# Optimization experiments

Measured on AMD Instinct MI355X. Metric: run time of the kernel, lower is better.

Reference implementation:

```python
import jax, jax.numpy as jnp
import numpy as np

B, L, D = 8, 2048, 1024
LN_EPS = 1e-5
WKV_EPS = 1e-8


def _ln(x, g, b):
    m = x.mean(-1, keepdims=True)
    v = x.var(-1, keepdims=True)  # biased var, matches torch LayerNorm
    return (x - m) * jax.lax.rsqrt(v + LN_EPS) * g + b


def _shift(x):
    # ZeroPad2d((0,0,1,-1)): x_prev[:, t] = x[:, t-1], x_prev[:, 0] = 0
    return jnp.pad(x, ((0, 0), (1, 0), (0, 0)))[:, :-1]


def _wkv(k, v, time_decay, time_first):
    # Faithful to the torch loop: t=0 uses exp(u + k0); t>0 decays prior state
    # (including the u-boosted first term) by exp(-exp(time_decay)).
    ew = jnp.exp(-jnp.exp(time_decay))  # [D]
    e0 = jnp.exp(time_first + k[:, 0])  # [B, D]
    a0 = e0 * v[:, 0]
    b0 = e0

    def step(carry, kv):
        a, b = carry
        kt, vt = kv
        ek = jnp.exp(kt)
        a = ew * a + ek * vt
        b = ew * b + ek
        return (a, b), a / (b + WKV_EPS)

    xs = (jnp.swapaxes(k[:, 1:], 0, 1), jnp.swapaxes(v[:, 1:], 0, 1))  # [L-1, B, D]
    _, outs = jax.lax.scan(step, (a0, b0), xs)
    out0 = (a0 / (b0 + WKV_EPS))[:, None]  # [B, 1, D]
    return jnp.concatenate([out0, jnp.swapaxes(outs, 0, 1)], axis=1)  # [B, L, D]


def setup_inputs() -> dict:
    key = jax.random.key(0)
    ks = jax.random.split(key, 10)
    s = 1.0 / np.sqrt(D)

    def w(k, shape, scale):
        return jax.random.normal(k, shape, jnp.float32) * scale

    return {
        "x": jax.random.normal(ks[0], (B, L, D), jnp.float32),
        "ln1_g": jnp.ones((D,), jnp.float32),
        "ln1_b": jnp.zeros((D,), jnp.float32),
        "Wk": w(ks[1], (D, D), s),
        "Wv": w(ks[2], (D, D), s),
        "Wr": w(ks[3], (D, D), s),
        "Wo": w(ks[4], (D, D), s),
        "time_decay": w(ks[5], (D,), 0.1),
        "time_first": w(ks[6], (D,), 0.1),
        "mix_k": jnp.full((D,), 0.5, jnp.float32),
        "mix_v": jnp.full((D,), 0.5, jnp.float32),
        "mix_r": jnp.full((D,), 0.5, jnp.float32),
        "ln2_g": jnp.ones((D,), jnp.float32),
        "ln2_b": jnp.zeros((D,), jnp.float32),
        "Wfk": w(ks[7], (D, 4 * D), s),
        "Wfv": w(ks[8], (4 * D, D), 1.0 / np.sqrt(4 * D)),
        "Wfr": w(ks[9], (D, D), s),
    }


def reference(x, ln1_g, ln1_b, Wk, Wv, Wr, Wo, time_decay, time_first,
              mix_k, mix_v, mix_r, ln2_g, ln2_b, Wfk, Wfv, Wfr):
    # --- time mixing ---
    xn = _ln(x, ln1_g, ln1_b)
    xp = _shift(xn)
    k = (xn * mix_k + xp * (1.0 - mix_k)) @ Wk
    v = (xn * mix_v + xp * (1.0 - mix_v)) @ Wv
    r = jax.nn.sigmoid((xn * mix_r + xp * (1.0 - mix_r)) @ Wr)
    wkv = _wkv(k, v, time_decay, time_first)
    x = x + (r * wkv) @ Wo
    # --- channel mixing ---
    yn = _ln(x, ln2_g, ln2_b)
    yp = _shift(yn)
    kk = jnp.square(jax.nn.relu((0.5 * yn + 0.5 * yp) @ Wfk))
    rr = jax.nn.sigmoid(yn @ Wfr)
    return x + rr * (kk @ Wfv)
```

## Files before the change

### kernel.cpp

```cpp
#include <hip/hip_runtime.h>
#include <hip/hip_bf16.h>
#include <stdint.h>

typedef __hip_bfloat16 bf16_t;
typedef __attribute__((ext_vector_type(8))) short bf16x8;
typedef __attribute__((ext_vector_type(4))) float f32x4;

#define DEV static __device__ __forceinline__

constexpr int kBB = 8, kL = 2048, kD = 1024;
constexpr int kM = kBB * kL;
constexpr int kSeg = 32, kP = 64;

DEV float bf2f(unsigned short u) { return __uint_as_float((unsigned)u << 16); }
DEV unsigned short f2bf(float f) {
  unsigned u = __float_as_uint(f);
  return (unsigned short)((u + 0x7fffu + ((u >> 16) & 1u)) >> 16);
}

DEV void gld16(const void* g, void* l) {
  const __attribute__((address_space(1))) unsigned* gp =
      (const __attribute__((address_space(1))) unsigned*)(uintptr_t)g;
  __attribute__((address_space(3))) unsigned* lp =
      (__attribute__((address_space(3))) unsigned*)(unsigned)(uintptr_t)l;
  __builtin_amdgcn_global_load_lds(gp, lp, 16, 0, 0);
}

__global__ __launch_bounds__(256) void k_transpose_cast(
    const float* __restrict__ W, bf16_t* __restrict__ Wt, int R, int C) {
  __shared__ float tile[32][33];
  const int bx = blockIdx.x * 32;
  const int by = blockIdx.y * 32;
  const int tx = threadIdx.x & 31, ty = threadIdx.x >> 5;
#pragma unroll
  for (int i = 0; i < 32; i += 8)
    tile[ty + i][tx] = W[(size_t)(by + ty + i) * C + (bx + tx)];
  __syncthreads();
#pragma unroll
  for (int i = 0; i < 32; i += 8)
    Wt[(size_t)(bx + ty + i) * R + (by + tx)] = __float2bfloat16(tile[tx][ty + i]);
}

__global__ __launch_bounds__(256) void k_ln_stats(
    const float* __restrict__ X, float* __restrict__ mean, float* __restrict__ rstd) {
  const int row = blockIdx.x * 4 + (threadIdx.x >> 6);
  const int lane = threadIdx.x & 63;
  const float4* xr = (const float4*)(X + (size_t)row * kD);
  float s = 0.f, s2 = 0.f;
#pragma unroll
  for (int i = 0; i < 4; ++i) {
    float4 v = xr[lane + 64 * i];
    s += v.x + v.y + v.z + v.w;
    s2 += v.x * v.x + v.y * v.y + v.z * v.z + v.w * v.w;
  }
#pragma unroll
  for (int off = 32; off > 0; off >>= 1) {
    s += __shfl_xor(s, off);
    s2 += __shfl_xor(s2, off);
  }
  if (lane == 0) {
    float m = s * (1.f / kD);
    float var = fmaxf(s2 * (1.f / kD) - m * m, 0.f);
    mean[row] = m;
    rstd[row] = rsqrtf(var + 1e-5f);
  }
}

__global__ __launch_bounds__(256) void k_ln_mix1(
    const float* __restrict__ X, const float* __restrict__ mean, const float* __restrict__ rstd,
    const float* __restrict__ g, const float* __restrict__ be,
    const float* __restrict__ mk, const float* __restrict__ mv, const float* __restrict__ mr,
    bf16_t* __restrict__ ok, bf16_t* __restrict__ ov, bf16_t* __restrict__ orr) {
  const int row = blockIdx.x;
  const int l = row & (kL - 1);
  const int i = threadIdx.x;
  const bool hp = (l != 0);
  const float m0 = mean[row], s0 = rstd[row];
  const float m1 = hp ? mean[row - 1] : 0.f;
  const float s1 = hp ? rstd[row - 1] : 0.f;
  float xa[4], pa[4] = {0.f, 0.f, 0.f, 0.f}, ga[4], ba[4], ka[4], va[4], ra[4];
  *(float4*)xa = ((const float4*)(X + (size_t)row * kD))[i];
  if (hp) *(float4*)pa = ((const float4*)(X + (size_t)(row - 1) * kD))[i];
  *(float4*)ga = ((const float4*)g)[i];
  *(float4*)ba = ((const float4*)be)[i];
  *(float4*)ka = ((const float4*)mk)[i];
  *(float4*)va = ((const float4*)mv)[i];
  *(float4*)ra = ((const float4*)mr)[i];
  ushort4 uk, uv, ur;
  unsigned short* pk = (unsigned short*)&uk;
  unsigned short* pv = (unsigned short*)&uv;
  unsigned short* pr = (unsigned short*)&ur;
#pragma unroll
  for (int c = 0; c < 4; ++c) {
    float xn = (xa[c] - m0) * s0 * ga[c] + ba[c];
    float xp = hp ? (pa[c] - m1) * s1 * ga[c] + ba[c] : 0.f;
    pk[c] = f2bf(xn * ka[c] + xp * (1.f - ka[c]));
    pv[c] = f2bf(xn * va[c] + xp * (1.f - va[c]));
    pr[c] = f2bf(xn * ra[c] + xp * (1.f - ra[c]));
  }
  ((ushort4*)(ok + (size_t)row * kD))[i] = uk;
  ((ushort4*)(ov + (size_t)row * kD))[i] = uv;
  ((ushort4*)(orr + (size_t)row * kD))[i] = ur;
}

__global__ __launch_bounds__(256) void k_ln_mix2(
    const float* __restrict__ X, const float* __restrict__ mean, const float* __restrict__ rstd,
    const float* __restrict__ g, const float* __restrict__ be,
    bf16_t* __restrict__ om, bf16_t* __restrict__ on) {
  const int row = blockIdx.x;
  const int l = row & (kL - 1);
  const int i = threadIdx.x;
  const bool hp = (l != 0);
  const float m0 = mean[row], s0 = rstd[row];
  const float m1 = hp ? mean[row - 1] : 0.f;
  const float s1 = hp ? rstd[row - 1] : 0.f;
  float xa[4], pa[4] = {0.f, 0.f, 0.f, 0.f}, ga[4], ba[4];
  *(float4*)xa = ((const float4*)(X + (size_t)row * kD))[i];
  if (hp) *(float4*)pa = ((const float4*)(X + (size_t)(row - 1) * kD))[i];
  *(float4*)ga = ((const float4*)g)[i];
  *(float4*)ba = ((const float4*)be)[i];
  ushort4 um, un;
  unsigned short* qm = (unsigned short*)&um;
  unsigned short* qn = (unsigned short*)&un;
#pragma unroll
  for (int c = 0; c < 4; ++c) {
    float yn = (xa[c] - m0) * s0 * ga[c] + ba[c];
    float yp = hp ? (pa[c] - m1) * s1 * ga[c] + ba[c] : 0.f;
    qm[c] = f2bf(0.5f * (yn + yp));
    qn[c] = f2bf(yn);
  }
  ((ushort4*)(om + (size_t)row * kD))[i] = um;
  ((ushort4*)(on + (size_t)row * kD))[i] = un;
}

__global__ __launch_bounds__(256) void k_wkv_seg(
    const unsigned short* __restrict__ kq, const unsigned short* __restrict__ vq,
    const float* __restrict__ td, const float* __restrict__ tf,
    float* __restrict__ segA, float* __restrict__ segB) {
  const int d = blockIdx.x * 256 + threadIdx.x;
  const int b = blockIdx.y;
  const int s = blockIdx.z;
  const float ew = __expf(-__expf(td[d]));
  const float uu = (s == 0) ? tf[d] : 0.f;
  const size_t base = ((size_t)b * kL + (size_t)s * kP) * kD + d;
  float a = 0.f, bb = 0.f;
  unsigned short kA[16], vA[16], kB[16], vB[16];
  auto pref = [&](unsigned short* ka, unsigned short* va, int c) {
    const size_t o0 = base + (size_t)c * 16 * kD;
#pragma unroll
    for (int j = 0; j < 16; ++j) {
      ka[j] = kq[o0 + (size_t)j * kD];
      va[j] = vq[o0 + (size_t)j * kD];
    }
  };
  auto comp = [&](const unsigned short* ka, const unsigned short* va, int c) {
#pragma unroll
    for (int j = 0; j < 16; ++j) {
      float kf = bf2f(ka[j]);
      if (s == 0 && c == 0 && j == 0) kf += uu;
      float ek = __expf(kf);
      a = ew * a + ek * bf2f(va[j]);
      bb = ew * bb + ek;
    }
  };
  pref(kA, vA, 0);
  pref(kB, vB, 1); comp(kA, vA, 0);
  pref(kA, vA, 2); comp(kB, vB, 1);
  pref(kB, vB, 3); comp(kA, vA, 2);
  comp(kB, vB, 3);
  const size_t sidx = ((size_t)b * kSeg + s) * kD + d;
  segA[sidx] = a;
  segB[sidx] = bb;
}

__global__ __launch_bounds__(256) void k_wkv_carry(
    const float* __restrict__ td,
    const float* __restrict__ segA, const float* __restrict__ segB,
    float* __restrict__ carA, float* __restrict__ carB) {
  const int d = blockIdx.x * 256 + threadIdx.x;
  const int b = blockIdx.y;
  const float ew = __expf(-__expf(td[d]));
  float ewP = ew;
#pragma unroll
  for (int i = 0; i < 6; ++i) ewP *= ewP;
  float ca = 0.f, cb = 0.f;
#pragma unroll 4
  for (int s = 0; s < kSeg; ++s) {
    const size_t idx = ((size_t)b * kSeg + s) * kD + d;
    carA[idx] = ca;
    carB[idx] = cb;
    ca = ewP * ca + segA[idx];
    cb = ewP * cb + segB[idx];
  }
}

__global__ __launch_bounds__(256) void k_wkv_out(
    const unsigned short* __restrict__ kq, const unsigned short* __restrict__ vq,
    const unsigned short* __restrict__ rq, const float* __restrict__ td,
    const float* __restrict__ tf, const float* __restrict__ carA,
    const float* __restrict__ carB, unsigned short* __restrict__ out) {
  const int d = blockIdx.x * 256 + threadIdx.x;
  const int b = blockIdx.y;
  const int s = blockIdx.z;
  const float ew = __expf(-__expf(td[d]));
  const float uu = (s == 0) ? tf[d] : 0.f;
  const size_t base = ((size_t)b * kL + (size_t)s * kP) * kD + d;
  const size_t sidx = ((size_t)b * kSeg + s) * kD + d;
  float a = carA[sidx], bb = carB[sidx];
  unsigned short kA[16], vA[16], rA[16], kB[16], vB[16], rB[16];
  auto pref = [&](unsigned short* ka, unsigned short* va, unsigned short* ra, int c) {
    const size_t o0 = base + (size_t)c * 16 * kD;
#pragma unroll
    for (int j = 0; j < 16; ++j) {
      ka[j] = kq[o0 + (size_t)j * kD];
      va[j] = vq[o0 + (size_t)j * kD];
      ra[j] = rq[o0 + (size_t)j * kD];
    }
  };
  auto comp = [&](const unsigned short* ka, const unsigned short* va,
                  const unsigned short* ra, int c) {
    const size_t o0 = base + (size_t)c * 16 * kD;
#pragma unroll
    for (int j = 0; j < 16; ++j) {
      float kf = bf2f(ka[j]);
      if (s == 0 && c == 0 && j == 0) kf += uu;
      float ek = __expf(kf);
      a = ew * a + ek * bf2f(va[j]);
      bb = ew * bb + ek;
      float y = a / (bb + 1e-8f);
      float sr = 1.f / (1.f + __expf(-bf2f(ra[j])));
      out[o0 + (size_t)j * kD] = f2bf(sr * y);
    }
  };
  pref(kA, vA, rA, 0);
  pref(kB, vB, rB, 1); comp(kA, vA, rA, 0);
  pref(kA, vA, rA, 2); comp(kB, vB, rB, 1);
  pref(kB, vB, rB, 3); comp(kA, vA, rA, 2);
  comp(kB, vB, rB, 3);
}

template <int EPI>
__global__ __launch_bounds__(512, 2) void gemmT(
    const bf16_t* __restrict__ A0, long strA, int lda,
    const bf16_t* __restrict__ B0, long strB, int ldb,
    bf16_t* __restrict__ Cb0, float* __restrict__ Cf, long strC,
    int N, int K, int nbx,
    const float* __restrict__ addf, const bf16_t* __restrict__ mulb) {
  __shared__ __align__(16) char lds[131072];
  const int z = blockIdx.z;
  const bf16_t* A = A0 + (size_t)z * strA;
  const bf16_t* Bt = B0 + (size_t)z * strB;
  const int nwg = gridDim.x;
  const int wg = (blockIdx.x & 7) * (nwg >> 3) + (blockIdx.x >> 3);
  const int by = wg / nbx, bx = wg - by * nbx;
  const long brow = (long)by * 256;
  const long bcol = (long)bx * 256;
  const int tid = threadIdx.x;
  const int lane = tid & 63;
  const int wid = tid >> 6;
  const int wr = wid >> 2, wc = wid & 3;

  f32x4 acc[8][4] = {};

  const int trow = tid >> 3;
  const int scol = ((tid & 7) * 16) ^ ((trow & 7) << 4);
  const char* Ag = (const char*)(A + (brow + trow) * (size_t)lda) + scol;
  const char* Bg = (const char*)(Bt + (bcol + trow) * (size_t)ldb) + scol;
  const long rsA = 64L * lda * 2;
  const long rsB = 64L * ldb * 2;

#define STAGE(kt, p)                                   \
  {                                                    \
    const long kb = (long)(kt) * 128;                  \
    char* Ld = lds + (p) * 65536 + tid * 16;           \
    gld16(Ag + kb, Ld);                                \
    gld16(Ag + kb + rsA, Ld + 8192);                   \
    gld16(Ag + kb + 2 * rsA, Ld + 16384);              \
    gld16(Ag + kb + 3 * rsA, Ld + 24576);              \
    gld16(Bg + kb, Ld + 32768);                        \
    gld16(Bg + kb + rsB, Ld + 40960);                  \
    gld16(Bg + kb + 2 * rsB, Ld + 49152);              \
    gld16(Bg + kb + 3 * rsB, Ld + 57344);              \
  }

  const int l16 = lane & 15, kq = lane >> 4;
  const int swz = (l16 & 7) << 4;
  const int oS0 = (kq * 16) ^ swz;
  const int oS1 = (64 + kq * 16) ^ swz;
  const char* Arow = lds + (wr * 128 + l16) * 128;
  const char* Brow = lds + 32768 + (wc * 64 + l16) * 128;

  bf16x8 aE[8], bE[4], aO[8], bO[4];
  const int NT = K >> 6;

  STAGE(0, 0) STAGE(1, 1)
  asm volatile("s_waitcnt vmcnt(8)" ::: "memory");
  __builtin_amdgcn_s_barrier();
#pragma unroll
  for (int m = 0; m < 8; ++m) aE[m] = *(const bf16x8*)(Arow + m * 2048 + oS0);
#pragma unroll
  for (int n = 0; n < 4; ++n) bE[n] = *(const bf16x8*)(Brow + n * 2048 + oS0);

  for (int t = 0; t < NT; ++t) {
    const int p = t & 1;
    const char* Ap = Arow + p * 65536;
    const char* Bp = Brow + p * 65536;
#pragma unroll
    for (int m = 0; m < 8; ++m) aO[m] = *(const bf16x8*)(Ap + m * 2048 + oS1);
#pragma unroll
    for (int n = 0; n < 4; ++n) bO[n] = *(const bf16x8*)(Bp + n * 2048 + oS1);
    __builtin_amdgcn_s_setprio(1);
#pragma unroll
    for (int m = 0; m < 8; ++m)
#pragma unroll
      for (int n = 0; n < 4; ++n)
        acc[m][n] = __builtin_amdgcn_mfma_f32_16x16x32_bf16(aE[m], bE[n], acc[m][n], 0, 0, 0);
    __builtin_amdgcn_s_setprio(0);
    asm volatile("s_waitcnt lgkmcnt(0)" ::: "memory");
    asm volatile("s_waitcnt vmcnt(0)" ::: "memory");
    __builtin_amdgcn_s_barrier();
    if (t + 2 < NT) STAGE(t + 2, p)
    if (t + 1 < NT) {
      const char* An = Arow + (1 - p) * 65536;
      const char* Bn = Brow + (1 - p) * 65536;
#pragma unroll
      for (int m = 0; m < 8; ++m) aE[m] = *(const bf16x8*)(An + m * 2048 + oS0);
#pragma unroll
      for (int n = 0; n < 4; ++n) bE[n] = *(const bf16x8*)(Bn + n * 2048 + oS0);
    }
    __builtin_amdgcn_s_setprio(1);
#pragma unroll
    for (int m = 0; m < 8; ++m)
#pragma unroll
      for (int n = 0; n < 4; ++n)
        acc[m][n] = __builtin_amdgcn_mfma_f32_16x16x32_bf16(aO[m], bO[n], acc[m][n], 0, 0, 0);
    __builtin_amdgcn_s_setprio(0);
  }
#undef STAGE

  bf16_t* Cb = Cb0 + (size_t)z * strC;
  const long orow = brow + wr * 128 + (lane >> 4) * 4;
  const long ocol = bcol + wc * 64 + l16;
#pragma unroll
  for (int m = 0; m < 8; ++m) {
#pragma unroll
    for (int reg = 0; reg < 4; ++reg) {
      const long r = orow + m * 16 + reg;
#pragma unroll
      for (int n = 0; n < 4; ++n) {
        const size_t idx = (size_t)r * N + ocol + n * 16;
        const float v = acc[m][n][reg];
        if constexpr (EPI == 0) {
          Cb[idx] = __float2bfloat16(v);
        } else if constexpr (EPI == 1) {
          Cf[idx] = addf[idx] + v;
        } else if constexpr (EPI == 2) {
          float u = v > 0.f ? v : 0.f;
          Cb[idx] = __float2bfloat16(u * u);
        } else if constexpr (EPI == 3) {
          Cb[idx] = __float2bfloat16(1.f / (1.f + __expf(-v)));
        } else if constexpr (EPI == 4) {
          Cf[idx] = v;
        } else {
          Cf[idx] = addf[idx] + __bfloat162float(mulb[idx]) * (Cf[idx] + v);
        }
      }
    }
  }
}

extern "C" void kernel_launch(void* const* d_in, const int* in_sizes, int n_in,
                              void* d_out, int out_size, void* d_ws, size_t ws_size,
                              hipStream_t stream) {
  const float* x    = (const float*)d_in[0];
  const float* ln1g = (const float*)d_in[1];
  const float* ln1b = (const float*)d_in[2];
  const float* Wk   = (const float*)d_in[3];
  const float* Wv   = (const float*)d_in[4];
  const float* Wr   = (const float*)d_in[5];
  const float* Wo   = (const float*)d_in[6];
  const float* td   = (const float*)d_in[7];
  const float* tf   = (const float*)d_in[8];
  const float* mk   = (const float*)d_in[9];
  const float* mv   = (const float*)d_in[10];
  const float* mr   = (const float*)d_in[11];
  const float* ln2g = (const float*)d_in[12];
  const float* ln2b = (const float*)d_in[13];
  const float* Wfk  = (const float*)d_in[14];
  const float* Wfv  = (const float*)d_in[15];
  const float* Wfr  = (const float*)d_in[16];

  char* ws = (char*)d_ws;
  const size_t MB = 1ull << 20;
  bf16_t* WkT  = (bf16_t*)(ws + 0 * MB);
  bf16_t* WvT  = (bf16_t*)(ws + 2 * MB);
  bf16_t* WrT  = (bf16_t*)(ws + 4 * MB);
  bf16_t* WoT  = (bf16_t*)(ws + 6 * MB);
  bf16_t* WfkT = (bf16_t*)(ws + 8 * MB);
  bf16_t* WfvT = (bf16_t*)(ws + 16 * MB);
  bf16_t* WfrT = (bf16_t*)(ws + 24 * MB);
  float* mean1 = (float*)(ws + 26 * MB);
  float* rstd1 = (float*)(ws + 26 * MB + 65536);
  float* mean2 = (float*)(ws + 26 * MB + 131072);
  float* rstd2 = (float*)(ws + 26 * MB + 196608);
  bf16_t* xk   = (bf16_t*)(ws + 28 * MB);
  bf16_t* xv   = (bf16_t*)(ws + 60 * MB);
  bf16_t* xr   = (bf16_t*)(ws + 92 * MB);
  bf16_t* kbuf = (bf16_t*)(ws + 124 * MB);
  bf16_t* vbuf = (bf16_t*)(ws + 156 * MB);
  bf16_t* rbuf = (bf16_t*)(ws + 188 * MB);
  float*  segA = (float*)(ws + 60 * MB);
  float*  segB = (float*)(ws + 61 * MB);
  float*  carA = (float*)(ws + 62 * MB);
  float*  carB = (float*)(ws + 63 * MB);
  bf16_t* rwkv = (bf16_t*)(ws + 92 * MB);
  float*  x1   = (float*)(ws + 28 * MB);
  bf16_t* rr   = (bf16_t*)(ws + 92 * MB);
  bf16_t* ynb  = (bf16_t*)(ws + 124 * MB);
  bf16_t* kk   = (bf16_t*)(ws + 124 * MB);
  bf16_t* ymix = (bf16_t*)(ws + 188 * MB);
  float*  out  = (float*)d_out;
  const long sX = (long)kM * kD;
  const long sW = (long)kD * kD;

  dim3 blk(256), blkg(512);
  k_transpose_cast<<<dim3(32, 32), blk, 0, stream>>>(Wk, WkT, 1024, 1024);
  k_transpose_cast<<<dim3(32, 32), blk, 0, stream>>>(Wv, WvT, 1024, 1024);
  k_transpose_cast<<<dim3(32, 32), blk, 0, stream>>>(Wr, WrT, 1024, 1024);
  k_transpose_cast<<<dim3(32, 32), blk, 0, stream>>>(Wo, WoT, 1024, 1024);
  k_transpose_cast<<<dim3(128, 32), blk, 0, stream>>>(Wfk, WfkT, 1024, 4096);
  k_transpose_cast<<<dim3(32, 128), blk, 0, stream>>>(Wfv, WfvT, 4096, 1024);
  k_transpose_cast<<<dim3(32, 32), blk, 0, stream>>>(Wfr, WfrT, 1024, 1024);

  k_ln_stats<<<kM / 4, blk, 0, stream>>>(x, mean1, rstd1);
  k_ln_mix1<<<kM, blk, 0, stream>>>(x, mean1, rstd1, ln1g, ln1b, mk, mv, mr, xk, xv, xr);
  gemmT<0><<<dim3(256, 1, 3), blkg, 0, stream>>>(xk, sX, 1024, WkT, sW, 1024,
      kbuf, nullptr, sX, 1024, 1024, 4, nullptr, nullptr);
  k_wkv_seg<<<dim3(4, 8, kSeg), blk, 0, stream>>>((const unsigned short*)kbuf,
      (const unsigned short*)vbuf, td, tf, segA, segB);
  k_wkv_carry<<<dim3(4, 8), blk, 0, stream>>>(td, segA, segB, carA, carB);
  k_wkv_out<<<dim3(4, 8, kSeg), blk, 0, stream>>>((const unsigned short*)kbuf,
      (const unsigned short*)vbuf, (const unsigned short*)rbuf, td, tf, carA, carB,
      (unsigned short*)rwkv);
  gemmT<1><<<256, blkg, 0, stream>>>(rwkv, 0, 1024, WoT, 0, 1024,
      nullptr, x1, 0, 1024, 1024, 4, x, nullptr);

  k_ln_stats<<<kM / 4, blk, 0, stream>>>(x1, mean2, rstd2);
  k_ln_mix2<<<kM, blk, 0, stream>>>(x1, mean2, rstd2, ln2g, ln2b, ymix, ynb);
  gemmT<3><<<256, blkg, 0, stream>>>(ynb, 0, 1024, WfrT, 0, 1024,
      rr, nullptr, 0, 1024, 1024, 4, nullptr, nullptr);
  for (int c = 0; c < 2; ++c) {
    gemmT<2><<<512, blkg, 0, stream>>>(ymix, 0, 1024, WfkT + (size_t)c * 2048 * 1024, 0, 1024,
        kk, nullptr, 0, 2048, 1024, 8, nullptr, nullptr);
    if (c == 0)
      gemmT<4><<<256, blkg, 0, stream>>>(kk, 0, 2048, WfvT + 0, 0, 4096,
          nullptr, out, 0, 1024, 2048, 4, nullptr, nullptr);
    else
      gemmT<6><<<256, blkg, 0, stream>>>(kk, 0, 2048, WfvT + 2048, 0, 4096,
          nullptr, out, 0, 1024, 2048, 4, x1, rr);
  }
}
```

Baseline: 654.1 us.

## Split GEMM k-loop into four barrier-separated phases with staggered half-tile prefetch

Restructures the 256x256 bf16 GEMM main loop into four phases per k-tile. Each phase loads one half of the A fragments plus the B fragments and runs 16 MFMAs. Global-to-LDS staging is split into two halves: one half for the next tile is issued early, the other half for tile t+2 is issued late, so loads spread across the loop and the full vmcnt(0) stall is avoided. Register pressure also drops, since the live A/B fragment registers shrink from 24 to 12. The cost is more barriers per iteration and tighter reliance on the hand-chosen vmcnt ordering between the two staging halves.

```diff
diff --git a/kernel.cpp b/kernel.cpp
--- a/kernel.cpp
+++ b/kernel.cpp
@@ -269,74 +269,100 @@
   const long rsA = 64L * lda * 2;
   const long rsB = 64L * ldb * 2;
 
-#define STAGE(kt, p)                                   \
-  {                                                    \
-    const long kb = (long)(kt) * 128;                  \
-    char* Ld = lds + (p) * 65536 + tid * 16;           \
-    gld16(Ag + kb, Ld);                                \
-    gld16(Ag + kb + rsA, Ld + 8192);                   \
-    gld16(Ag + kb + 2 * rsA, Ld + 16384);              \
-    gld16(Ag + kb + 3 * rsA, Ld + 24576);              \
-    gld16(Bg + kb, Ld + 32768);                        \
-    gld16(Bg + kb + rsB, Ld + 40960);                  \
-    gld16(Bg + kb + 2 * rsB, Ld + 49152);              \
-    gld16(Bg + kb + 3 * rsB, Ld + 57344);              \
-  }
+#define STG_FULL(kt, db) { const long kb = (long)(kt) * 128;       \
+    gld16(Ag + kb,           (db) + tid * 16);                     \
+    gld16(Ag + kb + rsA,     (db) + 8192 + tid * 16);              \
+    gld16(Ag + kb + 2 * rsA, (db) + 16384 + tid * 16);             \
+    gld16(Ag + kb + 3 * rsA, (db) + 24576 + tid * 16);             \
+    gld16(Bg + kb,           (db) + 32768 + tid * 16);             \
+    gld16(Bg + kb + rsB,     (db) + 40960 + tid * 16);             \
+    gld16(Bg + kb + 2 * rsB, (db) + 49152 + tid * 16);             \
+    gld16(Bg + kb + 3 * rsB, (db) + 57344 + tid * 16); }
+#define STG_HI(kt, db) { const long kb = (long)(kt) * 128;         \
+    gld16(Ag + kb + rsA,     (db) + 8192 + tid * 16);              \
+    gld16(Ag + kb + 3 * rsA, (db) + 24576 + tid * 16);             \
+    gld16(Bg + kb + 2 * rsB, (db) + 49152 + tid * 16);             \
+    gld16(Bg + kb + 3 * rsB, (db) + 57344 + tid * 16); }
+#define STG_LO(kt, db) { const long kb = (long)(kt) * 128;         \
+    gld16(Ag + kb,           (db) + tid * 16);                     \
+    gld16(Ag + kb + 2 * rsA, (db) + 16384 + tid * 16);             \
+    gld16(Bg + kb,           (db) + 32768 + tid * 16);             \
+    gld16(Bg + kb + rsB,     (db) + 40960 + tid * 16); }
 
   const int l16 = lane & 15, kq = lane >> 4;
   const int swz = (l16 & 7) << 4;
   const int oS0 = (kq * 16) ^ swz;
   const int oS1 = (64 + kq * 16) ^ swz;
-  const char* Arow = lds + (wr * 128 + l16) * 128;
-  const char* Brow = lds + 32768 + (wc * 64 + l16) * 128;
-
-  bf16x8 aE[8], bE[4], aO[8], bO[4];
+  const int ArowB = (wr * 128 + l16) * 128;
+  const int BrowB = 32768 + (wc * 64 + l16) * 128;
+
+  bf16x8 aF[4], aG[4], bF[4];
   const int NT = K >> 6;
 
-  STAGE(0, 0) STAGE(1, 1)
-  asm volatile("s_waitcnt vmcnt(8)" ::: "memory");
+  STG_FULL(0, lds)
+  if (NT > 1) {
+    STG_LO(1, lds + 65536)
+    asm volatile("s_waitcnt vmcnt(4)" ::: "memory");
+  } else {
+    asm volatile("s_waitcnt vmcnt(0)" ::: "memory");
+  }
   __builtin_amdgcn_s_barrier();
-#pragma unroll
-  for (int m = 0; m < 8; ++m) aE[m] = *(const bf16x8*)(Arow + m * 2048 + oS0);
-#pragma unroll
-  for (int n = 0; n < 4; ++n) bE[n] = *(const bf16x8*)(Brow + n * 2048 + oS0);
+
+#define PH_TAIL                                            \
+  __builtin_amdgcn_s_barrier();                            \
+  asm volatile("s_waitcnt lgkmcnt(0)" ::: "memory");       \
+  __builtin_amdgcn_sched_barrier(0);                       \
+  __builtin_amdgcn_s_setprio(1);
+
+#define MFMA16(AR, MB)                                     \
+  _Pragma("unroll")                                        \
+  for (int i = 0; i < 4; ++i)                              \
+    _Pragma("unroll")                                      \
+    for (int n = 0; n < 4; ++n)                            \
+      acc[(MB) + i][n] = __builtin_amdgcn_mfma_f32_16x16x32_bf16(AR[i], bF[n], acc[(MB) + i][n], 0, 0, 0);
 
   for (int t = 0; t < NT; ++t) {
-    const int p = t & 1;
-    const char* Ap = Arow + p * 65536;
-    const char* Bp = Brow + p * 65536;
-#pragma unroll
-    for (int m = 0; m < 8; ++m) aO[m] = *(const bf16x8*)(Ap + m * 2048 + oS1);
-#pragma unroll
-    for (int n = 0; n < 4; ++n) bO[n] = *(const bf16x8*)(Bp + n * 2048 + oS1);
-    __builtin_amdgcn_s_setprio(1);
-#pragma unroll
-    for (int m = 0; m < 8; ++m)
-#pragma unroll
-      for (int n = 0; n < 4; ++n)
-        acc[m][n] = __builtin_amdgcn_mfma_f32_16x16x32_bf16(aE[m], bE[n], acc[m][n], 0, 0, 0);
+    const char* bc = lds + (t & 1) * 65536;
+    char* bn = lds + ((t + 1) & 1) * 65536;
+    char* bw = lds + (t & 1) * 65536;
+#pragma unroll
+    for (int i = 0; i < 4; ++i) aF[i] = *(const bf16x8*)(bc + ArowB + i * 2048 + oS0);
+#pragma unroll
+    for (int n = 0; n < 4; ++n) bF[n] = *(const bf16x8*)(bc + BrowB + n * 2048 + oS0);
+    if (t + 1 < NT) STG_HI(t + 1, bn)
+    PH_TAIL
+    MFMA16(aF, 0)
     __builtin_amdgcn_s_setprio(0);
-    asm volatile("s_waitcnt lgkmcnt(0)" ::: "memory");
-    asm volatile("s_waitcnt vmcnt(0)" ::: "memory");
     __builtin_amdgcn_s_barrier();
-    if (t + 2 < NT) STAGE(t + 2, p)
-    if (t + 1 < NT) {
-      const char* An = Arow + (1 - p) * 65536;
-      const char* Bn = Brow + (1 - p) * 65536;
-#pragma unroll
-      for (int m = 0; m < 8; ++m) aE[m] = *(const bf16x8*)(An + m * 2048 + oS0);
-#pragma unroll
-      for (int n = 0; n < 4; ++n) bE[n] = *(const bf16x8*)(Bn + n * 2048 + oS0);
-    }
-    __builtin_amdgcn_s_setprio(1);
-#pragma unroll
-    for (int m = 0; m < 8; ++m)
-#pragma unroll
-      for (int n = 0; n < 4; ++n)
-        acc[m][n] = __builtin_amdgcn_mfma_f32_16x16x32_bf16(aO[m], bO[n], acc[m][n], 0, 0, 0);
+#pragma unroll
+    for (int i = 0; i < 4; ++i) aG[i] = *(const bf16x8*)(bc + ArowB + 8192 + i * 2048 + oS0);
+    PH_TAIL
+    MFMA16(aG, 4)
     __builtin_amdgcn_s_setprio(0);
-  }
-#undef STAGE
+    __builtin_amdgcn_s_barrier();
+#pragma unroll
+    for (int i = 0; i < 4; ++i) aF[i] = *(const bf16x8*)(bc + ArowB + i * 2048 + oS1);
+#pragma unroll
+    for (int n = 0; n < 4; ++n) bF[n] = *(const bf16x8*)(bc + BrowB + n * 2048 + oS1);
+    PH_TAIL
+    MFMA16(aF, 0)
+    __builtin_amdgcn_s_setprio(0);
+    __builtin_amdgcn_s_barrier();
+#pragma unroll
+    for (int i = 0; i < 4; ++i) aG[i] = *(const bf16x8*)(bc + ArowB + 8192 + i * 2048 + oS1);
+    if (t + 2 < NT) STG_LO(t + 2, bw)
+    PH_TAIL
+    MFMA16(aG, 4)
+    __builtin_amdgcn_s_setprio(0);
+    if (t + 2 < NT) { asm volatile("s_waitcnt vmcnt(4)" ::: "memory"); }
+    else            { asm volatile("s_waitcnt vmcnt(0)" ::: "memory"); }
+    __builtin_amdgcn_s_barrier();
+  }
+#undef STG_FULL
+#undef STG_HI
+#undef STG_LO
+#undef PH_TAIL
+#undef MFMA16
 
   bf16_t* Cb = Cb0 + (size_t)z * strC;
   const long orow = brow + wr * 128 + (lane >> 4) * 4;
```

After: 676.0 us. +3.4%, slower.

## Fuse LayerNorm stats into mix kernels and add sched barriers in GEMM loop

Applied to the files above, without the earlier changes.

Removes the separate LayerNorm statistics kernels. Each mix kernel now computes the mean and rstd for its own row and the previous row, using wave shuffles followed by a shared-memory reduction. This saves two kernel launches and one extra read pass over the activations, at the cost of recomputing the previous row's statistics. It also inserts sched_barrier fences before the MFMA blocks in the GEMM main loop to stop the compiler from interleaving LDS reads with the matrix ops.

```diff
diff --git a/kernel.cpp b/kernel.cpp
--- a/kernel.cpp
+++ b/kernel.cpp
@@ -41,46 +41,39 @@
     Wt[(size_t)(bx + ty + i) * R + (by + tx)] = __float2bfloat16(tile[tx][ty + i]);
 }
 
-__global__ __launch_bounds__(256) void k_ln_stats(
-    const float* __restrict__ X, float* __restrict__ mean, float* __restrict__ rstd) {
-  const int row = blockIdx.x * 4 + (threadIdx.x >> 6);
-  const int lane = threadIdx.x & 63;
-  const float4* xr = (const float4*)(X + (size_t)row * kD);
-  float s = 0.f, s2 = 0.f;
-#pragma unroll
-  for (int i = 0; i < 4; ++i) {
-    float4 v = xr[lane + 64 * i];
-    s += v.x + v.y + v.z + v.w;
-    s2 += v.x * v.x + v.y * v.y + v.z * v.z + v.w * v.w;
-  }
-#pragma unroll
-  for (int off = 32; off > 0; off >>= 1) {
-    s += __shfl_xor(s, off);
-    s2 += __shfl_xor(s2, off);
-  }
-  if (lane == 0) {
-    float m = s * (1.f / kD);
-    float var = fmaxf(s2 * (1.f / kD) - m * m, 0.f);
-    mean[row] = m;
-    rstd[row] = rsqrtf(var + 1e-5f);
-  }
-}
-
-__global__ __launch_bounds__(256) void k_ln_mix1(
-    const float* __restrict__ X, const float* __restrict__ mean, const float* __restrict__ rstd,
-    const float* __restrict__ g, const float* __restrict__ be,
+__global__ __launch_bounds__(256) void k_ln1f(
+    const float* __restrict__ X, const float* __restrict__ g, const float* __restrict__ be,
     const float* __restrict__ mk, const float* __restrict__ mv, const float* __restrict__ mr,
     bf16_t* __restrict__ ok, bf16_t* __restrict__ ov, bf16_t* __restrict__ orr) {
   const int row = blockIdx.x;
   const int l = row & (kL - 1);
   const int i = threadIdx.x;
   const bool hp = (l != 0);
-  const float m0 = mean[row], s0 = rstd[row];
-  const float m1 = hp ? mean[row - 1] : 0.f;
-  const float s1 = hp ? rstd[row - 1] : 0.f;
-  float xa[4], pa[4] = {0.f, 0.f, 0.f, 0.f}, ga[4], ba[4], ka[4], va[4], ra[4];
+  float xa[4], pa[4] = {0.f, 0.f, 0.f, 0.f};
   *(float4*)xa = ((const float4*)(X + (size_t)row * kD))[i];
   if (hp) *(float4*)pa = ((const float4*)(X + (size_t)(row - 1) * kD))[i];
+  float s0 = xa[0] + xa[1] + xa[2] + xa[3];
+  float q0 = xa[0] * xa[0] + xa[1] * xa[1] + xa[2] * xa[2] + xa[3] * xa[3];
+  float s1 = pa[0] + pa[1] + pa[2] + pa[3];
+  float q1 = pa[0] * pa[0] + pa[1] * pa[1] + pa[2] * pa[2] + pa[3] * pa[3];
+#pragma unroll
+  for (int off = 32; off > 0; off >>= 1) {
+    s0 += __shfl_xor(s0, off); q0 += __shfl_xor(q0, off);
+    s1 += __shfl_xor(s1, off); q1 += __shfl_xor(q1, off);
+  }
+  __shared__ float red[4][4];
+  const int wid = i >> 6, lane = i & 63;
+  if (lane == 0) { red[wid][0] = s0; red[wid][1] = q0; red[wid][2] = s1; red[wid][3] = q1; }
+  __syncthreads();
+  s0 = red[0][0] + red[1][0] + red[2][0] + red[3][0];
+  q0 = red[0][1] + red[1][1] + red[2][1] + red[3][1];
+  s1 = red[0][2] + red[1][2] + red[2][2] + red[3][2];
+  q1 = red[0][3] + red[1][3] + red[2][3] + red[3][3];
+  const float m0 = s0 * (1.f / kD);
+  const float r0 = rsqrtf(fmaxf(q0 * (1.f / kD) - m0 * m0, 0.f) + 1e-5f);
+  const float m1 = s1 * (1.f / kD);
+  const float r1 = rsqrtf(fmaxf(q1 * (1.f / kD) - m1 * m1, 0.f) + 1e-5f);
+  float ga[4], ba[4], ka[4], va[4], ra[4];
   *(float4*)ga = ((const float4*)g)[i];
   *(float4*)ba = ((const float4*)be)[i];
   *(float4*)ka = ((const float4*)mk)[i];
@@ -92,8 +85,8 @@
   unsigned short* pr = (unsigned short*)&ur;
 #pragma unroll
   for (int c = 0; c < 4; ++c) {
-    float xn = (xa[c] - m0) * s0 * ga[c] + ba[c];
-    float xp = hp ? (pa[c] - m1) * s1 * ga[c] + ba[c] : 0.f;
+    float xn = (xa[c] - m0) * r0 * ga[c] + ba[c];
+    float xp = hp ? (pa[c] - m1) * r1 * ga[c] + ba[c] : 0.f;
     pk[c] = f2bf(xn * ka[c] + xp * (1.f - ka[c]));
     pv[c] = f2bf(xn * va[c] + xp * (1.f - va[c]));
     pr[c] = f2bf(xn * ra[c] + xp * (1.f - ra[c]));
@@ -103,20 +96,38 @@
   ((ushort4*)(orr + (size_t)row * kD))[i] = ur;
 }
 
-__global__ __launch_bounds__(256) void k_ln_mix2(
-    const float* __restrict__ X, const float* __restrict__ mean, const float* __restrict__ rstd,
-    const float* __restrict__ g, const float* __restrict__ be,
+__global__ __launch_bounds__(256) void k_ln2f(
+    const float* __restrict__ X, const float* __restrict__ g, const float* __restrict__ be,
     bf16_t* __restrict__ om, bf16_t* __restrict__ on) {
   const int row = blockIdx.x;
   const int l = row & (kL - 1);
   const int i = threadIdx.x;
   const bool hp = (l != 0);
-  const float m0 = mean[row], s0 = rstd[row];
-  const float m1 = hp ? mean[row - 1] : 0.f;
-  const float s1 = hp ? rstd[row - 1] : 0.f;
-  float xa[4], pa[4] = {0.f, 0.f, 0.f, 0.f}, ga[4], ba[4];
+  float xa[4], pa[4] = {0.f, 0.f, 0.f, 0.f};
   *(float4*)xa = ((const float4*)(X + (size_t)row * kD))[i];
   if (hp) *(float4*)pa = ((const float4*)(X + (size_t)(row - 1) * kD))[i];
+  float s0 = xa[0] + xa[1] + xa[2] + xa[3];
+  float q0 = xa[0] * xa[0] + xa[1] * xa[1] + xa[2] * xa[2] + xa[3] * xa[3];
+  float s1 = pa[0] + pa[1] + pa[2] + pa[3];
+  float q1 = pa[0] * pa[0] + pa[1] * pa[1] + pa[2] * pa[2] + pa[3] * pa[3];
+#pragma unroll
+  for (int off = 32; off > 0; off >>= 1) {
+    s0 += __shfl_xor(s0, off); q0 += __shfl_xor(q0, off);
+    s1 += __shfl_xor(s1, off); q1 += __shfl_xor(q1, off);
+  }
+  __shared__ float red[4][4];
+  const int wid = i >> 6, lane = i & 63;
+  if (lane == 0) { red[wid][0] = s0; red[wid][1] = q0; red[wid][2] = s1; red[wid][3] = q1; }
+  __syncthreads();
+  s0 = red[0][0] + red[1][0] + red[2][0] + red[3][0];
+  q0 = red[0][1] + red[1][1] + red[2][1] + red[3][1];
+  s1 = red[0][2] + red[1][2] + red[2][2] + red[3][2];
+  q1 = red[0][3] + red[1][3] + red[2][3] + red[3][3];
+  const float m0 = s0 * (1.f / kD);
+  const float r0 = rsqrtf(fmaxf(q0 * (1.f / kD) - m0 * m0, 0.f) + 1e-5f);
+  const float m1 = s1 * (1.f / kD);
+  const float r1 = rsqrtf(fmaxf(q1 * (1.f / kD) - m1 * m1, 0.f) + 1e-5f);
+  float ga[4], ba[4];
   *(float4*)ga = ((const float4*)g)[i];
   *(float4*)ba = ((const float4*)be)[i];
   ushort4 um, un;
@@ -124,8 +135,8 @@
   unsigned short* qn = (unsigned short*)&un;
 #pragma unroll
   for (int c = 0; c < 4; ++c) {
-    float yn = (xa[c] - m0) * s0 * ga[c] + ba[c];
-    float yp = hp ? (pa[c] - m1) * s1 * ga[c] + ba[c] : 0.f;
+    float yn = (xa[c] - m0) * r0 * ga[c] + ba[c];
+    float yp = hp ? (pa[c] - m1) * r1 * ga[c] + ba[c] : 0.f;
     qm[c] = f2bf(0.5f * (yn + yp));
     qn[c] = f2bf(yn);
   }
@@ -309,6 +320,7 @@
     for (int m = 0; m < 8; ++m) aO[m] = *(const bf16x8*)(Ap + m * 2048 + oS1);
 #pragma unroll
     for (int n = 0; n < 4; ++n) bO[n] = *(const bf16x8*)(Bp + n * 2048 + oS1);
+    __builtin_amdgcn_sched_barrier(0);
     __builtin_amdgcn_s_setprio(1);
 #pragma unroll
     for (int m = 0; m < 8; ++m)
@@ -328,6 +340,7 @@
 #pragma unroll
       for (int n = 0; n < 4; ++n) bE[n] = *(const bf16x8*)(Bn + n * 2048 + oS0);
     }
+    __builtin_amdgcn_sched_barrier(0);
     __builtin_amdgcn_s_setprio(1);
 #pragma unroll
     for (int m = 0; m < 8; ++m)
@@ -399,10 +412,6 @@
   bf16_t* WfkT = (bf16_t*)(ws + 8 * MB);
   bf16_t* WfvT = (bf16_t*)(ws + 16 * MB);
   bf16_t* WfrT = (bf16_t*)(ws + 24 * MB);
-  float* mean1 = (float*)(ws + 26 * MB);
-  float* rstd1 = (float*)(ws + 26 * MB + 65536);
-  float* mean2 = (float*)(ws + 26 * MB + 131072);
-  float* rstd2 = (float*)(ws + 26 * MB + 196608);
   bf16_t* xk   = (bf16_t*)(ws + 28 * MB);
   bf16_t* xv   = (bf16_t*)(ws + 60 * MB);
   bf16_t* xr   = (bf16_t*)(ws + 92 * MB);
@@ -432,8 +441,7 @@
   k_transpose_cast<<<dim3(32, 128), blk, 0, stream>>>(Wfv, WfvT, 4096, 1024);
   k_transpose_cast<<<dim3(32, 32), blk, 0, stream>>>(Wfr, WfrT, 1024, 1024);
 
-  k_ln_stats<<<kM / 4, blk, 0, stream>>>(x, mean1, rstd1);
-  k_ln_mix1<<<kM, blk, 0, stream>>>(x, mean1, rstd1, ln1g, ln1b, mk, mv, mr, xk, xv, xr);
+  k_ln1f<<<kM, blk, 0, stream>>>(x, ln1g, ln1b, mk, mv, mr, xk, xv, xr);
   gemmT<0><<<dim3(256, 1, 3), blkg, 0, stream>>>(xk, sX, 1024, WkT, sW, 1024,
       kbuf, nullptr, sX, 1024, 1024, 4, nullptr, nullptr);
   k_wkv_seg<<<dim3(4, 8, kSeg), blk, 0, stream>>>((const unsigned short*)kbuf,
@@ -445,8 +453,7 @@
   gemmT<1><<<256, blkg, 0, stream>>>(rwkv, 0, 1024, WoT, 0, 1024,
       nullptr, x1, 0, 1024, 1024, 4, x, nullptr);
 
-  k_ln_stats<<<kM / 4, blk, 0, stream>>>(x1, mean2, rstd2);
-  k_ln_mix2<<<kM, blk, 0, stream>>>(x1, mean2, rstd2, ln2g, ln2b, ymix, ynb);
+  k_ln2f<<<kM, blk, 0, stream>>>(x1, ln2g, ln2b, ymix, ynb);
   gemmT<3><<<256, blkg, 0, stream>>>(ynb, 0, 1024, WfrT, 0, 1024,
       rr, nullptr, 0, 1024, 1024, 4, nullptr, nullptr);
   for (int c = 0; c < 2; ++c) {
```

After: 642.1 us. Within noise of the previous version (-1.8%).
